# Kernel tuning notes

Measured on AMD Instinct MI355X. Metric: run time of the kernel, lower is better.

The kernel has to match this reference:

```python
import jax, jax.numpy as jnp
import numpy as np

B, L, E, V = 256, 256, 100, 100000  # trees, leaves per tree, embed_size, vocab
T = L - 1                           # compose steps per tree (left fold)


def setup_inputs() -> dict:
    key = jax.random.key(0)
    k1, k2, k3, k4 = jax.random.split(key, 4)
    token_ids = jax.random.randint(k1, (B, L), 0, V)
    # Left-fold composition plan shared across the batch (buffer layout:
    # slots [0,L) hold leaf embeddings, slot L+t holds the step-t result).
    # step 0: compose(leaf0, leaf1); step t>0: compose(result_{t-1}, leaf_{t+1})
    comp_left = jnp.concatenate([jnp.array([0], jnp.int32),
                                 (L + jnp.arange(T - 1)).astype(jnp.int32)])
    comp_left = jnp.broadcast_to(comp_left, (B, T))
    comp_right = jnp.broadcast_to(jnp.arange(1, L, dtype=jnp.int32), (B, T))
    embeddings = jax.random.normal(k2, (V, E), jnp.float32)
    W1 = jax.random.normal(k3, (E, 2 * E), jnp.float32) * (1.0 / np.sqrt(2 * E))
    b1 = jnp.zeros((E,), jnp.float32)
    W2 = jax.random.normal(k4, (1, E), jnp.float32) * (1.0 / np.sqrt(E))
    b2 = jnp.zeros((1,), jnp.float32)
    return dict(token_ids=token_ids, comp_left=comp_left, comp_right=comp_right,
                embeddings=embeddings, W1=W1, b1=b1, W2=W2, b2=b2)


def reference(token_ids, comp_left, comp_right, embeddings, W1, b1, W2, b2):
    leaf = embeddings[token_ids]                                  # [B, L, E]
    buf = jnp.concatenate([leaf, jnp.zeros((B, T, E), leaf.dtype)], axis=1)  # [B, L+T, E]
    bidx = jnp.arange(B)

    def step(buf, xs):
        t, li, ri = xs                                            # li, ri: [B]
        left = buf[bidx, li]                                      # [B, E]
        right = buf[bidx, ri]                                     # [B, E]
        ab = jnp.concatenate([left, right], axis=-1)              # [B, 2E]
        out = jnp.tanh(ab @ W1.T + b1)                            # compose
        buf = buf.at[bidx, L + t].set(out)
        return buf, None

    xs = (jnp.arange(T), comp_left.T, comp_right.T)
    buf, _ = jax.lax.scan(step, buf, xs)
    root = buf[:, L + T - 1]                                      # [B, E]
    return jax.nn.sigmoid(root @ W2.T + b2)                       # [B, 1]
```

## Files before the change

kernel.cpp:

```cpp
#include <hip/hip_runtime.h>
#include <math.h>


#define Bc 256
#define Lc 256
#define Ec 100
#define Tc 255
#define W1cols 200

#define RL(v, k) __int_as_float(__builtin_amdgcn_readlane(__float_as_int(v), (k)))
#define RF(x)    __builtin_amdgcn_readfirstlane(x)

#define REP25(X) X(0) X(1) X(2) X(3) X(4) X(5) X(6) X(7) X(8) X(9) X(10) X(11) X(12) \
                 X(13) X(14) X(15) X(16) X(17) X(18) X(19) X(20) X(21) X(22) X(23) X(24)
#define DECLWC(j) float wA##j, wB##j;
#define LOADWC(j) { wA##j = rowA[j]; wB##j = rowB[j]; }
#define CM2(a,b) { const float ra_ = RL(sv,(a)), rb_ = RL(sv,(b)); \
    accA0 = fmaf(ra_, wA##a, accA0); accB0 = fmaf(ra_, wB##a, accB0); \
    accA1 = fmaf(rb_, wA##b, accA1); accB1 = fmaf(rb_, wB##b, accB1); }
#define CM1(a) { const float ra_ = RL(sv,(a)); \
    accA0 = fmaf(ra_, wA##a, accA0); accB0 = fmaf(ra_, wB##a, accB0); }
#define CMALL CM2(0,1) CM2(2,3) CM2(4,5) CM2(6,7) CM2(8,9) CM2(10,11) CM2(12,13) \
              CM2(14,15) CM2(16,17) CM2(18,19) CM2(20,21) CM2(22,23) CM1(24)

__device__ __noinline__ float slow_dot(const float* rp, const float* wr) {
    float a0 = 0.f, a1 = 0.f, a2 = 0.f, a3 = 0.f;
    for (int qq = 0; qq < 25; ++qq) {
        float4 h4 = *(const float4*)(rp + 4 * qq);
        float4 w4 = *(const float4*)(wr + 4 * qq);
        a0 = fmaf(w4.x, h4.x, a0); a1 = fmaf(w4.y, h4.y, a1);
        a2 = fmaf(w4.z, h4.z, a2); a3 = fmaf(w4.w, h4.w, a3);
    }
    return (a0 + a1) + (a2 + a3);
}

__global__ __launch_bounds__(512, 2)
void fused(const int* __restrict__ token_ids,
           const int* __restrict__ comp_left,
           const int* __restrict__ comp_right,
           const float* __restrict__ emb,
           const float* __restrict__ W1,
           const float* __restrict__ b1,
           const float* __restrict__ W2,
           const float* __restrict__ b2,
           float* __restrict__ out)
{
    const int b    = blockIdx.x;
    const int tid  = threadIdx.x;
    const int wv   = tid >> 6;
    const int l    = tid & 63;
    const bool cons = (wv < 4);
    const int q    = wv & 3;
    const int lc   = (l < 50) ? l : 49;

    __shared__ float hist[Tc * Ec];
    __shared__ float part[2][4][Ec];
    __shared__ float cpart[8][4][Ec];
    __shared__ int2  ccS[Tc];
    __shared__ int   tokRS[Tc], tokLS[Tc];
    __shared__ float red[4];

    for (int i = tid; i < Tc; i += 512) {
        const int cl = comp_left [b * Tc + i];
        const int cr = comp_right[b * Tc + i];
        ccS[i]   = make_int2(cl, cr);
        tokRS[i] = (cr < Lc) ? token_ids[b * Lc + cr] : -1;
        tokLS[i] = (cl < Lc) ? token_ids[b * Lc + cl] : -1;
    }

    const int kofs = (cons ? 0 : Ec) + 25 * q;
    const float* rowA = W1 + (size_t)lc * W1cols + kofs;
    const float* rowB = W1 + (size_t)(lc + 50) * W1cols + kofs;
    REP25(DECLWC)
    REP25(LOADWC)
    const float b1eA = (!cons && q == 0) ? b1[lc] : 0.f;
    const float b1eB = (!cons && q == 0) ? b1[lc + 50] : 0.f;

    __syncthreads();

    float vh = 0.f;
    int2  cc = make_int2(0, 0);
    float vA0 = 0.f, vA1 = 0.f;
    int   tk0 = -1, tk1 = -1;

    if (cons) {
        cc = ccS[0];
    } else {
        for (int t = 0; t < 2; ++t) {
            const int tk = RF(tokRS[t]);
            float sv = 0.f;
            if (tk >= 0 && l < 25) sv = emb[(size_t)tk * Ec + 25 * q + l];
            float accA0 = b1eA, accA1 = 0.f, accB0 = b1eB, accB1 = 0.f;
            if (tk >= 0) { CMALL }
            if (l < 50) {
                cpart[t][q][lc]      = accA0 + accA1;
                cpart[t][q][lc + 50] = accB0 + accB1;
            }
        }
        tk0 = (2 < Tc) ? RF(tokRS[2]) : -1;
        if (tk0 >= 0 && l < 25) vA0 = emb[(size_t)tk0 * Ec + 25 * q + l];
        tk1 = (3 < Tc) ? RF(tokRS[3]) : -1;
        if (tk1 >= 0 && l < 25) vA1 = emb[(size_t)tk1 * Ec + 25 * q + l];
    }

#define BARRIER asm volatile("s_waitcnt lgkmcnt(0)\n\ts_barrier" ::: "memory");

#define TICK(I, PPc, PAR)                                                     \
{                                                                             \
    const int i_ = (I);                                                       \
    if (cons) {                                                               \
        const int tc = i_ - 1;                                                \
        if (tc >= 0) {                                                        \
            __builtin_amdgcn_s_setprio(1);                                    \
            const int li = RF(cc.x);                                          \
            const int ri = RF(cc.y);                                          \
                       \
            float cp0 = 0.f, cp1 = 0.f, cp2 = 0.f, cp3 = 0.f;                 \
            if (l < 25) {                                                     \
                const int r_ = 25 * q + l;                                    \
                cp0 = cpart[tc & 7][0][r_]; cp1 = cpart[tc & 7][1][r_];       \
                cp2 = cpart[tc & 7][2][r_]; cp3 = cpart[tc & 7][3][r_];       \
            }                                                                 \
            float sv = 0.f;                                                   \
            if (tc >= 1 && li == Lc + tc - 1) {                               \
                sv = vh;                              \
            } else if (li >= Lc) {                                            \
                const int n = li - Lc;                                        \
                if (n < tc && l < 25) sv = hist[n * Ec + 25 * q + l];         \
            } else {                                                          \
                const int tl = RF(tokLS[tc]);                                 \
                if (tl >= 0 && l < 25) sv = emb[(size_t)tl * Ec + 25 * q + l];\
            }                                                                 \
            float accA0 = 0.f, accA1 = 0.f, accB0 = 0.f, accB1 = 0.f;         \
            CMALL                                                             \
            if (l < 50) {                                                     \
                part[PPc][q][lc]      = accA0 + accA1;                        \
                part[PPc][q][lc + 50] = accB0 + accB1;                        \
            }                                                                 \
            BARRIER                                                           \
            if (l < 25) {                                                     \
                const int r = 25 * q + l;                                     \
                float x = ((part[PPc][0][r] + part[PPc][1][r]) +              \
                           (part[PPc][2][r] + part[PPc][3][r])) +             \
                          ((cp0 + cp1) + (cp2 + cp3));                        \
                if (ri >= Lc) {                                               \
                    const int n = ri - Lc;                                    \
                    if (n < tc) x += slow_dot(&hist[n * Ec],                  \
                                              W1 + (size_t)r * W1cols + Ec);  \
                }                                                             \
                const float u = __expf(2.f * x);                              \
                vh = 1.f - 2.f / (u + 1.f);         \
                hist[tc * Ec + r] = vh;               \
            }                                                                 \
            __builtin_amdgcn_s_setprio(0);                                    \
            if (tc + 1 < Tc) cc = ccS[tc + 1];                                \
        } else {                                                              \
            BARRIER                                                           \
        }                                                                     \
    } else {                                                                  \
        const int t = i_ + 2;                                                 \
        if (t < Tc) {                                                         \
            const float sv  = (PAR) ? vA1 : vA0;      \
            const int   tkc = (PAR) ? tk1 : tk0;                              \
            const int   tn  = t + 2;                    \
            const int tknew = (tn < Tc) ? RF(tokRS[tn]) : -1;                 \
            float nv = 0.f;                                                   \
            if (tknew >= 0 && l < 25) nv = emb[(size_t)tknew * Ec + 25 * q + l];\
            if (PAR) { vA1 = nv; tk1 = tknew; } else { vA0 = nv; tk0 = tknew; }\
            float accA0 = b1eA, accA1 = 0.f, accB0 = b1eB, accB1 = 0.f;       \
            if (tkc >= 0) { CMALL }                                           \
            if (l < 50) {                                                     \
                cpart[t & 7][q][lc]      = accA0 + accA1;                     \
                cpart[t & 7][q][lc + 50] = accB0 + accB1;                     \
            }                                                                 \
        }                                                                     \
        BARRIER                                                               \
    }                                                                         \
}

    #pragma unroll 1
    for (int i2 = 0; i2 < 256; i2 += 2) {
        TICK(i2,     1, 0)
        TICK(i2 + 1, 0, 1)
    }
#undef TICK
#undef BARRIER

    if (cons) {
        float pv = 0.f;
        if (l < 25) pv = W2[25 * q + l] * vh;
        #pragma unroll
        for (int off = 32; off > 0; off >>= 1) pv += __shfl_down(pv, off, 64);
        if (l == 0) red[q] = pv;
    }
    __syncthreads();
    if (tid == 0)
        out[b] = 1.f / (1.f + __expf(-((red[0] + red[1]) + (red[2] + red[3]) + b2[0])));
}

extern "C" void kernel_launch(void* const* d_in, const int* in_sizes, int n_in,
                              void* d_out, int out_size, void* d_ws, size_t ws_size,
                              hipStream_t stream) {
    const int*   token_ids  = (const int*)  d_in[0];
    const int*   comp_left  = (const int*)  d_in[1];
    const int*   comp_right = (const int*)  d_in[2];
    const float* emb        = (const float*)d_in[3];
    const float* W1         = (const float*)d_in[4];
    const float* b1         = (const float*)d_in[5];
    const float* W2         = (const float*)d_in[6];
    const float* b2         = (const float*)d_in[7];
    float*       out        = (float*)d_out;

    fused<<<Bc, 512, 0, stream>>>(token_ids, comp_left, comp_right,
                                  emb, W1, b1, W2, b2, out);
}
```

Baseline: 131.2 us.

## Use padded LDS history with broadcast float4 reads and packed FMAs in the compose step

The recurrent consumer waves stop broadcasting the left operand lane by lane with readlane. Instead they read it from a padded shared-memory history (row stride 112, quarter stride 28), using float4 broadcast loads feeding v_pk_fma_f32 on float2-packed W1 columns. Leaf operands are read directly from global embeddings, and the right-child fallback dot product is adapted to the padded layout. The goal is to shorten the serial per-step latency of the dependent readlane/FMA chain. In exchange, the register fast path for the previous result is dropped, each step now waits on an LDS read, and shared memory use grows.

```diff
diff --git a/kernel.cpp b/kernel.cpp
--- a/kernel.cpp
+++ b/kernel.cpp
@@ -7,14 +7,16 @@
 #define Ec 100
 #define Tc 255
 #define W1cols 200
+#define HS 112
 
 #define RL(v, k) __int_as_float(__builtin_amdgcn_readlane(__float_as_int(v), (k)))
 #define RF(x)    __builtin_amdgcn_readfirstlane(x)
 
 #define REP25(X) X(0) X(1) X(2) X(3) X(4) X(5) X(6) X(7) X(8) X(9) X(10) X(11) X(12) \
                  X(13) X(14) X(15) X(16) X(17) X(18) X(19) X(20) X(21) X(22) X(23) X(24)
-#define DECLWC(j) float wA##j, wB##j;
-#define LOADWC(j) { wA##j = rowA[j]; wB##j = rowB[j]; }
+
+#define DECLWP(j) float wA##j, wB##j;
+#define LOADWP(j) { wA##j = prowA[j]; wB##j = prowB[j]; }
 #define CM2(a,b) { const float ra_ = RL(sv,(a)), rb_ = RL(sv,(b)); \
     accA0 = fmaf(ra_, wA##a, accA0); accB0 = fmaf(ra_, wB##a, accB0); \
     accA1 = fmaf(rb_, wA##b, accA1); accB1 = fmaf(rb_, wB##b, accB1); }
@@ -23,15 +25,27 @@
 #define CMALL CM2(0,1) CM2(2,3) CM2(4,5) CM2(6,7) CM2(8,9) CM2(10,11) CM2(12,13) \
               CM2(14,15) CM2(16,17) CM2(18,19) CM2(20,21) CM2(22,23) CM1(24)
 
-__device__ __noinline__ float slow_dot(const float* rp, const float* wr) {
-    float a0 = 0.f, a1 = 0.f, a2 = 0.f, a3 = 0.f;
-    for (int qq = 0; qq < 25; ++qq) {
-        float4 h4 = *(const float4*)(rp + 4 * qq);
-        float4 w4 = *(const float4*)(wr + 4 * qq);
-        a0 = fmaf(w4.x, h4.x, a0); a1 = fmaf(w4.y, h4.y, a1);
-        a2 = fmaf(w4.z, h4.z, a2); a3 = fmaf(w4.w, h4.w, a3);
-    }
-    return (a0 + a1) + (a2 + a3);
+#define DECLWC(j) float2 Wc##j;
+#define LOADWC(j) { Wc##j = make_float2(crowA[j], crowB[j]); }
+#define PKLO(A,W,H) asm("v_pk_fma_f32 %0, %1, %2, %0 op_sel:[0,0,0] op_sel_hi:[1,0,1]" \
+                        : "+v"(A) : "v"(W), "v"(H));
+#define PKHI(A,W,H) asm("v_pk_fma_f32 %0, %1, %2, %0 op_sel:[0,1,0] op_sel_hi:[1,1,1]" \
+                        : "+v"(A) : "v"(W), "v"(H));
+#define CQUAD(qq, a,b,c,d) { \
+    const float4 h4_ = *(const float4*)(hb + 4*(qq)); \
+    const float2 hlo_ = make_float2(h4_.x, h4_.y); \
+    const float2 hhi_ = make_float2(h4_.z, h4_.w); \
+    PKLO(ac0, Wc##a, hlo_) PKHI(ac1, Wc##b, hlo_) \
+    PKLO(ac2, Wc##c, hhi_) PKHI(ac3, Wc##d, hhi_) }
+#define LEAF(j) { const float hj_ = g[j]; \
+    accA = fmaf(Wc##j.x, hj_, accA); accB = fmaf(Wc##j.y, hj_, accB); }
+
+__device__ __noinline__ float slow_dot_g(const float* hg, const float* wr) {
+    float a0 = 0.f;
+    for (int qq = 0; qq < 4; ++qq)
+        for (int j = 0; j < 25; ++j)
+            a0 = fmaf(hg[28 * qq + j], wr[25 * qq + j], a0);
+    return a0;
 }
 
 __global__ __launch_bounds__(512, 2)
@@ -53,7 +67,7 @@
     const int q    = wv & 3;
     const int lc   = (l < 50) ? l : 49;
 
-    __shared__ float hist[Tc * Ec];
+    __shared__ __align__(16) float hist[Tc * HS];
     __shared__ float part[2][4][Ec];
     __shared__ float cpart[8][4][Ec];
     __shared__ int2  ccS[Tc];
@@ -68,11 +82,14 @@
         tokLS[i] = (cl < Lc) ? token_ids[b * Lc + cl] : -1;
     }
 
-    const int kofs = (cons ? 0 : Ec) + 25 * q;
-    const float* rowA = W1 + (size_t)lc * W1cols + kofs;
-    const float* rowB = W1 + (size_t)(lc + 50) * W1cols + kofs;
+    const float* crowA = W1 + (size_t)lc * W1cols + 25 * q;
+    const float* crowB = W1 + (size_t)(lc + 50) * W1cols + 25 * q;
     REP25(DECLWC)
-    REP25(LOADWC)
+    const float* prowA = W1 + (size_t)lc * W1cols + Ec + 25 * q;
+    const float* prowB = W1 + (size_t)(lc + 50) * W1cols + Ec + 25 * q;
+    REP25(DECLWP)
+    if (cons) { REP25(LOADWC) }
+    else      { REP25(LOADWP) }
     const float b1eA = (!cons && q == 0) ? b1[lc] : 0.f;
     const float b1eB = (!cons && q == 0) ? b1[lc + 50] : 0.f;
 
@@ -114,28 +131,39 @@
             __builtin_amdgcn_s_setprio(1);                                    \
             const int li = RF(cc.x);                                          \
             const int ri = RF(cc.y);                                          \
-                       \
+                                                          \
             float cp0 = 0.f, cp1 = 0.f, cp2 = 0.f, cp3 = 0.f;                 \
             if (l < 25) {                                                     \
                 const int r_ = 25 * q + l;                                    \
                 cp0 = cpart[tc & 7][0][r_]; cp1 = cpart[tc & 7][1][r_];       \
                 cp2 = cpart[tc & 7][2][r_]; cp3 = cpart[tc & 7][3][r_];       \
             }                                                                 \
-            float sv = 0.f;                                                   \
-            if (tc >= 1 && li == Lc + tc - 1) {                               \
-                sv = vh;                              \
-            } else if (li >= Lc) {                                            \
+            float accA = 0.f, accB = 0.f;                                     \
+            if (li >= Lc) {                                                   \
                 const int n = li - Lc;                                        \
-                if (n < tc && l < 25) sv = hist[n * Ec + 25 * q + l];         \
-            } else {                                                          \
+                if (n < tc) {            \
+                    const float* hb = &hist[n * HS + 28 * q];                 \
+                    float2 ac0 = make_float2(0.f, 0.f), ac1 = ac0;            \
+                    float2 ac2 = ac0, ac3 = ac0;                              \
+                    CQUAD(0, 0,1,2,3)   CQUAD(1, 4,5,6,7)                     \
+                    CQUAD(2, 8,9,10,11) CQUAD(3, 12,13,14,15)                 \
+                    CQUAD(4, 16,17,18,19) CQUAD(5, 20,21,22,23)               \
+                    const float h24_ = hb[24];                                \
+                    accA = fmaf(Wc24.x, h24_,                                 \
+                                (ac0.x + ac1.x) + (ac2.x + ac3.x));           \
+                    accB = fmaf(Wc24.y, h24_,                                 \
+                                (ac0.y + ac1.y) + (ac2.y + ac3.y));           \
+                }                          \
+            } else {                    \
                 const int tl = RF(tokLS[tc]);                                 \
-                if (tl >= 0 && l < 25) sv = emb[(size_t)tl * Ec + 25 * q + l];\
-            }                                                                 \
-            float accA0 = 0.f, accA1 = 0.f, accB0 = 0.f, accB1 = 0.f;         \
-            CMALL                                                             \
+                if (tl >= 0) {                                                \
+                    const float* g = emb + (size_t)tl * Ec + 25 * q;          \
+                    REP25(LEAF)                                               \
+                }                                                             \
+            }                                                                 \
             if (l < 50) {                                                     \
-                part[PPc][q][lc]      = accA0 + accA1;                        \
-                part[PPc][q][lc + 50] = accB0 + accB1;                        \
+                part[PPc][q][lc]      = accA;                                 \
+                part[PPc][q][lc + 50] = accB;                                 \
             }                                                                 \
             BARRIER                                                           \
             if (l < 25) {                                                     \
@@ -143,14 +171,14 @@
                 float x = ((part[PPc][0][r] + part[PPc][1][r]) +              \
                            (part[PPc][2][r] + part[PPc][3][r])) +             \
                           ((cp0 + cp1) + (cp2 + cp3));                        \
-                if (ri >= Lc) {                                               \
-                    const int n = ri - Lc;                                    \
-                    if (n < tc) x += slow_dot(&hist[n * Ec],                  \
-                                              W1 + (size_t)r * W1cols + Ec);  \
+                if (ri >= Lc) {            \
+                    const int n2 = ri - Lc;                                   \
+                    if (n2 < tc) x += slow_dot_g(&hist[n2 * HS],              \
+                                                 W1 + (size_t)r * W1cols + Ec);\
                 }                                                             \
                 const float u = __expf(2.f * x);                              \
                 vh = 1.f - 2.f / (u + 1.f);         \
-                hist[tc * Ec + r] = vh;               \
+                hist[tc * HS + 28 * q + l] = vh;                              \
             }                                                                 \
             __builtin_amdgcn_s_setprio(0);                                    \
             if (tc + 1 < Tc) cc = ccS[tc + 1];                                \
```

New measurement: 144.7 us. +10.2%, slower.
